# Kernel optimization log

Measured on AMD Instinct MI355X. Metric: run time of the kernel, lower is better.

Reference implementation:

```python
import jax, jax.numpy as jnp
import numpy as np

NEG = -10000.0
START_ID, END_ID, PAD_ID = 0, 1, 2
B, S, T = 512, 512, 128


def setup_inputs() -> dict:
    key = jax.random.key(0)
    k1, k2, k3, k4 = jax.random.split(key, 4)
    x = jax.random.normal(k1, (B, S, T), dtype=jnp.float32)
    tags = jax.random.randint(k2, (B, S), 0, T)
    # prefix-ones mask; lengths in [1, S-2] so the gather at mask.sum(1) is in-range
    lengths = jax.random.randint(k3, (B,), 1, S - 1)
    mask = (jnp.arange(S)[None, :] < lengths[:, None]).astype(jnp.float32)
    # torch xavier_normal_ on (T, T): std = sqrt(2 / (T + T))
    std = (2.0 / (T + T)) ** 0.5
    transition = std * jax.random.normal(k4, (T, T), dtype=jnp.float32)
    return {"x": x, "tags": tags, "mask": mask, "transition": transition}


def _crf_forward(x, mask, transition):
    # forward algorithm: log partition function, shape (B,)
    b, s, t = x.shape
    alpha0 = jnp.full((b, t), NEG, dtype=x.dtype).at[:, START_ID].set(0.0)

    def step(alpha, inp):
        x_t, m_t = inp  # (B,T), (B,)
        # scores[b, next, prev] = alpha[b, prev] + x_t[b, next] + transition[next, prev]
        scores = alpha[:, None, :] + x_t[:, :, None] + transition[None, :, :]
        new = jax.scipy.special.logsumexp(scores, axis=2)  # (B,T)
        m = m_t[:, None]
        return new * m + alpha * (1.0 - m), None

    alpha, _ = jax.lax.scan(step, alpha0, (jnp.swapaxes(x, 0, 1), jnp.swapaxes(mask, 0, 1)))
    return jax.scipy.special.logsumexp(alpha + transition[END_ID], axis=1)


def _crf_score(x, tags, mask, transition):
    # gold path score, shape (B,) — emission at t is paired with tags[:, t+1]
    b, s, t = x.shape
    em = jnp.take_along_axis(x[:, : s - 1], tags[:, 1:s, None], axis=2)[..., 0]  # (B,S-1)
    tr = transition[tags[:, 1:s], tags[:, : s - 1]]  # (B,S-1)
    score = jnp.sum((em + tr) * mask[:, : s - 1], axis=1)
    last_idx = mask.sum(axis=1).astype(jnp.int32)  # (B,)
    last_tag = jnp.take_along_axis(tags, last_idx[:, None], axis=1)[:, 0]
    return score + transition[END_ID, last_tag]


def reference(x, tags, mask, transition):
    fwd_score = _crf_forward(x, mask, transition)
    gold_score = _crf_score(x, tags, mask, transition)
    return jnp.mean(fwd_score - gold_score)
```

## Files before the change

### kernel.cpp

```cpp
#include <hip/hip_runtime.h>

#define NTAG 128
#define SEQ 512
#define NBATCH 512
#define END_ID 1

typedef _Float16 h2 __attribute__((ext_vector_type(2)));
typedef __fp16 fp16x2 __attribute__((ext_vector_type(2)));
typedef uint u32x32 __attribute__((ext_vector_type(32)));

__device__ __forceinline__ float bcast0(float v) {
  return __int_as_float(__builtin_amdgcn_readfirstlane(__float_as_int(v)));
}
__device__ __forceinline__ uint pack2(float a, float b) {
  fp16x2 h = __builtin_amdgcn_cvt_pkrtz(a, b);
  return __builtin_bit_cast(uint, h);
}
__device__ __forceinline__ h2 as_h2(uint u) { return __builtin_bit_cast(h2, u); }

#if __has_builtin(__builtin_amdgcn_fdot2)
#define FDOT2(pu, eu, acc) acc = __builtin_amdgcn_fdot2(as_h2(pu), as_h2(eu), acc, false)
#else
#define FDOT2(pu, eu, acc) do { h2 _p = as_h2(pu), _e = as_h2(eu); \
  acc = fmaf((float)_p.x, (float)_e.x, fmaf((float)_p.y, (float)_e.y, acc)); } while (0)
#endif

__global__ __launch_bounds__(64, 1) void crf_kernel(
    const float* __restrict__ x,
    const int*   __restrict__ tags,
    const float* __restrict__ mask,
    const float* __restrict__ trans,
    float* __restrict__ ws)
{
  const int b    = blockIdx.x;
  const int lane = threadIdx.x;

  __shared__ alignas(16) uint p_lds[64];

  const float* xb   = x    + (size_t)b * SEQ * NTAG;
  const float* mrow = mask + (size_t)b * SEQ;
  const int*   trow = tags + (size_t)b * SEQ;

  float msum = 0.f;
  #pragma unroll
  for (int i = 0; i < SEQ / 64; ++i) msum += mrow[lane + i * 64];
  #pragma unroll
  for (int off = 1; off < 64; off <<= 1) msum += __shfl_xor(msum, off);
  const int len = (int)msum;

  u32x32 eL0, eL1, eH0, eH1;
  {
    const float4* r0 = (const float4*)(trans + (size_t)(2 * lane) * NTAG);
    const float4* r1 = (const float4*)(trans + (size_t)(2 * lane + 1) * NTAG);
    #pragma unroll
    for (int k4 = 0; k4 < 16; ++k4) {
      float4 lo = r0[k4], hi = r1[k4];
      eL0[2 * k4 + 0] = pack2(__expf(lo.x), __expf(lo.y));
      eL0[2 * k4 + 1] = pack2(__expf(lo.z), __expf(lo.w));
      eH0[2 * k4 + 0] = pack2(__expf(hi.x), __expf(hi.y));
      eH0[2 * k4 + 1] = pack2(__expf(hi.z), __expf(hi.w));
    }
    #pragma unroll
    for (int k4 = 16; k4 < 32; ++k4) {
      float4 lo = r0[k4], hi = r1[k4];
      eL1[2 * (k4 - 16) + 0] = pack2(__expf(lo.x), __expf(lo.y));
      eL1[2 * (k4 - 16) + 1] = pack2(__expf(lo.z), __expf(lo.w));
      eH1[2 * (k4 - 16) + 0] = pack2(__expf(hi.x), __expf(hi.y));
      eH1[2 * (k4 - 16) + 1] = pack2(__expf(hi.z), __expf(hi.w));
    }
  }

  float a_lo = (lane == 0) ? 0.f : -10000.f;
  float a_hi = -10000.f;
  float2 xt = ((const float2*)xb)[lane];

  for (int t = 0; t < len; ++t) {
    const float m = bcast0(a_lo);
    const float p0 = fminf(__expf(a_lo - m), 60000.f);
    const float p1 = fminf(__expf(a_hi - m), 60000.f);
    p_lds[lane] = pack2(p0, p1);

    const float2 xn = ((const float2*)(xb + (size_t)(t + 1) * NTAG))[lane];

    float qL = 0.f, qH = 0.f;
    const uint4* p4 = (const uint4*)p_lds;
    #pragma unroll
    for (int c = 0; c < 8; ++c) {
      uint4 pv = p4[c];
      FDOT2(pv.x, eL0[4 * c + 0], qL); FDOT2(pv.x, eH0[4 * c + 0], qH);
      FDOT2(pv.y, eL0[4 * c + 1], qL); FDOT2(pv.y, eH0[4 * c + 1], qH);
      FDOT2(pv.z, eL0[4 * c + 2], qL); FDOT2(pv.z, eH0[4 * c + 2], qH);
      FDOT2(pv.w, eL0[4 * c + 3], qL); FDOT2(pv.w, eH0[4 * c + 3], qH);
    }
    #pragma unroll
    for (int c = 8; c < 16; ++c) {
      uint4 pv = p4[c];
      FDOT2(pv.x, eL1[4 * (c - 8) + 0], qL); FDOT2(pv.x, eH1[4 * (c - 8) + 0], qH);
      FDOT2(pv.y, eL1[4 * (c - 8) + 1], qL); FDOT2(pv.y, eH1[4 * (c - 8) + 1], qH);
      FDOT2(pv.z, eL1[4 * (c - 8) + 2], qL); FDOT2(pv.z, eH1[4 * (c - 8) + 2], qH);
      FDOT2(pv.w, eL1[4 * (c - 8) + 3], qL); FDOT2(pv.w, eH1[4 * (c - 8) + 3], qH);
    }

    a_lo = xt.x + m + __logf(qL);
    a_hi = xt.y + m + __logf(qH);
    xt = xn;
  }

  const float2 te = ((const float2*)(trans + END_ID * NTAG))[lane];
  const float v_lo = a_lo + te.x;
  const float v_hi = a_hi + te.y;
  float m2 = fmaxf(v_lo, v_hi);
  #pragma unroll
  for (int off = 1; off < 64; off <<= 1) m2 = fmaxf(m2, __shfl_xor(m2, off));
  float s = __expf(v_lo - m2) + __expf(v_hi - m2);
  #pragma unroll
  for (int off = 1; off < 64; off <<= 1) s += __shfl_xor(s, off);
  const float fwd = m2 + __logf(s);

  float g = 0.f;
  for (int i = lane; i < len; i += 64) {
    const int tn = trow[i + 1];
    const int tp = trow[i];
    g += xb[(size_t)i * NTAG + tn] + trans[tn * NTAG + tp];
  }
  #pragma unroll
  for (int off = 1; off < 64; off <<= 1) g += __shfl_xor(g, off);

  if (lane == 0) {
    const float gold = g + trans[END_ID * NTAG + trow[len]];
    ws[b] = fwd - gold;
  }
}

__global__ void reduce_kernel(const float* __restrict__ ws, float* __restrict__ out) {
  __shared__ float sm[8];
  const int tid = threadIdx.x;
  float v = ws[tid];
  #pragma unroll
  for (int off = 1; off < 64; off <<= 1) v += __shfl_xor(v, off);
  if ((tid & 63) == 0) sm[tid >> 6] = v;
  __syncthreads();
  if (tid == 0) {
    float s = 0.f;
    #pragma unroll
    for (int w = 0; w < 8; ++w) s += sm[w];
    out[0] = s * (1.0f / 512.0f);
  }
}

extern "C" void kernel_launch(void* const* d_in, const int* in_sizes, int n_in,
                              void* d_out, int out_size, void* d_ws, size_t ws_size,
                              hipStream_t stream) {
  const float* x     = (const float*)d_in[0];
  const int*   tags  = (const int*)d_in[1];
  const float* mask  = (const float*)d_in[2];
  const float* trans = (const float*)d_in[3];
  float*       ws    = (float*)d_ws;

  crf_kernel<<<NBATCH, 64, 0, stream>>>(x, tags, mask, trans, ws);
  reduce_kernel<<<1, 512, 0, stream>>>(ws, (float*)d_out);
}
```

Measured before the change: 424.1 us.

## Broadcast probabilities via readlane instead of LDS and work in log2 domain

Removes the LDS staging of the packed probability vector and broadcasts each lane's packed fp16 pair to the wave with 64 v_readlane instructions feeding the dot products. The recurrence state moves to base-2 log space so the per-step exp and log become native exp2/log2 with one fma, dropping the scale multiplies. This avoids an LDS write-then-read round trip on the serial critical path each step. In exchange it issues 64 readlanes per step, each a cross-lane move that may carry its own latency and limit issue rate.

Result: faster. 386.6 us (-8.8%).

```diff
diff --git a/kernel.cpp b/kernel.cpp
--- a/kernel.cpp
+++ b/kernel.cpp
@@ -9,6 +9,9 @@
 typedef __fp16 fp16x2 __attribute__((ext_vector_type(2)));
 typedef uint u32x32 __attribute__((ext_vector_type(32)));
 
+#define LOG2E 1.4426950408889634f
+#define LN2   0.6931471805599453f
+
 __device__ __forceinline__ float bcast0(float v) {
   return __int_as_float(__builtin_amdgcn_readfirstlane(__float_as_int(v)));
 }
@@ -17,6 +20,21 @@
   return __builtin_bit_cast(uint, h);
 }
 __device__ __forceinline__ h2 as_h2(uint u) { return __builtin_bit_cast(h2, u); }
+
+__device__ __forceinline__ float fast_exp2(float x) {
+#if __has_builtin(__builtin_amdgcn_exp2f)
+  return __builtin_amdgcn_exp2f(x);
+#else
+  return exp2f(x);
+#endif
+}
+__device__ __forceinline__ float fast_log2(float x) {
+#if __has_builtin(__builtin_amdgcn_logf)
+  return __builtin_amdgcn_logf(x);
+#else
+  return log2f(x);
+#endif
+}
 
 #if __has_builtin(__builtin_amdgcn_fdot2)
 #define FDOT2(pu, eu, acc) acc = __builtin_amdgcn_fdot2(as_h2(pu), as_h2(eu), acc, false)
@@ -34,8 +52,6 @@
 {
   const int b    = blockIdx.x;
   const int lane = threadIdx.x;
-
-  __shared__ alignas(16) uint p_lds[64];
 
   const float* xb   = x    + (size_t)b * SEQ * NTAG;
   const float* mrow = mask + (size_t)b * SEQ;
@@ -55,56 +71,49 @@
     #pragma unroll
     for (int k4 = 0; k4 < 16; ++k4) {
       float4 lo = r0[k4], hi = r1[k4];
-      eL0[2 * k4 + 0] = pack2(__expf(lo.x), __expf(lo.y));
-      eL0[2 * k4 + 1] = pack2(__expf(lo.z), __expf(lo.w));
-      eH0[2 * k4 + 0] = pack2(__expf(hi.x), __expf(hi.y));
-      eH0[2 * k4 + 1] = pack2(__expf(hi.z), __expf(hi.w));
+      eL0[2 * k4 + 0] = pack2(fast_exp2(lo.x * LOG2E), fast_exp2(lo.y * LOG2E));
+      eL0[2 * k4 + 1] = pack2(fast_exp2(lo.z * LOG2E), fast_exp2(lo.w * LOG2E));
+      eH0[2 * k4 + 0] = pack2(fast_exp2(hi.x * LOG2E), fast_exp2(hi.y * LOG2E));
+      eH0[2 * k4 + 1] = pack2(fast_exp2(hi.z * LOG2E), fast_exp2(hi.w * LOG2E));
     }
     #pragma unroll
     for (int k4 = 16; k4 < 32; ++k4) {
       float4 lo = r0[k4], hi = r1[k4];
-      eL1[2 * (k4 - 16) + 0] = pack2(__expf(lo.x), __expf(lo.y));
-      eL1[2 * (k4 - 16) + 1] = pack2(__expf(lo.z), __expf(lo.w));
-      eH1[2 * (k4 - 16) + 0] = pack2(__expf(hi.x), __expf(hi.y));
-      eH1[2 * (k4 - 16) + 1] = pack2(__expf(hi.z), __expf(hi.w));
+      eL1[2 * (k4 - 16) + 0] = pack2(fast_exp2(lo.x * LOG2E), fast_exp2(lo.y * LOG2E));
+      eL1[2 * (k4 - 16) + 1] = pack2(fast_exp2(lo.z * LOG2E), fast_exp2(lo.w * LOG2E));
+      eH1[2 * (k4 - 16) + 0] = pack2(fast_exp2(hi.x * LOG2E), fast_exp2(hi.y * LOG2E));
+      eH1[2 * (k4 - 16) + 1] = pack2(fast_exp2(hi.z * LOG2E), fast_exp2(hi.w * LOG2E));
     }
   }
 
-  float a_lo = (lane == 0) ? 0.f : -10000.f;
-  float a_hi = -10000.f;
+  float A_lo = (lane == 0) ? 0.f : -14427.f;
+  float A_hi = -14427.f;
   float2 xt = ((const float2*)xb)[lane];
 
   for (int t = 0; t < len; ++t) {
-    const float m = bcast0(a_lo);
-    const float p0 = fminf(__expf(a_lo - m), 60000.f);
-    const float p1 = fminf(__expf(a_hi - m), 60000.f);
-    p_lds[lane] = pack2(p0, p1);
+    const float M = bcast0(A_lo);
+    const uint pk = pack2(fminf(fast_exp2(A_lo - M), 60000.f),
+                          fminf(fast_exp2(A_hi - M), 60000.f));
 
     const float2 xn = ((const float2*)(xb + (size_t)(t + 1) * NTAG))[lane];
 
     float qL = 0.f, qH = 0.f;
-    const uint4* p4 = (const uint4*)p_lds;
     #pragma unroll
-    for (int c = 0; c < 8; ++c) {
-      uint4 pv = p4[c];
-      FDOT2(pv.x, eL0[4 * c + 0], qL); FDOT2(pv.x, eH0[4 * c + 0], qH);
-      FDOT2(pv.y, eL0[4 * c + 1], qL); FDOT2(pv.y, eH0[4 * c + 1], qH);
-      FDOT2(pv.z, eL0[4 * c + 2], qL); FDOT2(pv.z, eH0[4 * c + 2], qH);
-      FDOT2(pv.w, eL0[4 * c + 3], qL); FDOT2(pv.w, eH0[4 * c + 3], qH);
-    }
-    #pragma unroll
-    for (int c = 8; c < 16; ++c) {
-      uint4 pv = p4[c];
-      FDOT2(pv.x, eL1[4 * (c - 8) + 0], qL); FDOT2(pv.x, eH1[4 * (c - 8) + 0], qH);
-      FDOT2(pv.y, eL1[4 * (c - 8) + 1], qL); FDOT2(pv.y, eH1[4 * (c - 8) + 1], qH);
-      FDOT2(pv.z, eL1[4 * (c - 8) + 2], qL); FDOT2(pv.z, eH1[4 * (c - 8) + 2], qH);
-      FDOT2(pv.w, eL1[4 * (c - 8) + 3], qL); FDOT2(pv.w, eH1[4 * (c - 8) + 3], qH);
+    for (int c = 0; c < 64; ++c) {
+      const uint pc = (uint)__builtin_amdgcn_readlane((int)pk, c);
+      const uint el = (c < 32) ? eL0[c] : eL1[c - 32];
+      const uint eh = (c < 32) ? eH0[c] : eH1[c - 32];
+      FDOT2(pc, el, qL);
+      FDOT2(pc, eh, qH);
     }
 
-    a_lo = xt.x + m + __logf(qL);
-    a_hi = xt.y + m + __logf(qH);
+    A_lo = fmaf(xt.x, LOG2E, M + fast_log2(qL));
+    A_hi = fmaf(xt.y, LOG2E, M + fast_log2(qH));
     xt = xn;
   }
+
+  const float a_lo = A_lo * LN2;
+  const float a_hi = A_hi * LN2;
 
   const float2 te = ((const float2*)(trans + END_ID * NTAG))[lane];
   const float v_lo = a_lo + te.x;
@@ -112,10 +121,10 @@
   float m2 = fmaxf(v_lo, v_hi);
   #pragma unroll
   for (int off = 1; off < 64; off <<= 1) m2 = fmaxf(m2, __shfl_xor(m2, off));
-  float s = __expf(v_lo - m2) + __expf(v_hi - m2);
+  float s = fast_exp2((v_lo - m2) * LOG2E) + fast_exp2((v_hi - m2) * LOG2E);
   #pragma unroll
   for (int off = 1; off < 64; off <<= 1) s += __shfl_xor(s, off);
-  const float fwd = m2 + __logf(s);
+  const float fwd = m2 + fast_log2(s) * LN2;
 
   float g = 0.f;
   for (int i = lane; i < len; i += 64) {
```
